# Optimization experiments

Measured on AMD Instinct MI355X. Metric: run time of the kernel, lower is better.

Reference implementation:

```python
import jax, jax.numpy as jnp
import numpy as np

N_NODES = 100000


def gcn_conv(x, src, dst, W, b, n):
    # PyG GCNConv: x' = D^-1/2 (A + I) D^-1/2 (x W) + b
    h = x @ W  # [N, out] transform first (cheaper when out < in)
    loop = jnp.arange(n, dtype=src.dtype)
    s = jnp.concatenate([src, loop])
    d = jnp.concatenate([dst, loop])
    deg = jax.ops.segment_sum(jnp.ones_like(s, dtype=h.dtype), d, num_segments=n)
    dinv = jnp.where(deg > 0, jax.lax.rsqrt(deg), 0.0)
    norm = dinv[s] * dinv[d]  # [E+N]
    msg = h[s] * norm[:, None]  # [E+N, out]
    agg = jax.ops.segment_sum(msg, d, num_segments=n)
    return agg + b


def setup_inputs() -> dict:
    key = jax.random.key(0)
    ks = jax.random.split(key, 12)
    n, E, labels = N_NODES, 1600000, 128
    edges = jax.random.randint(ks[0], (2, E), 0, n, dtype=jnp.int64)
    features = jax.random.normal(ks[1], (n, labels), dtype=jnp.float32)

    def kaiming(k, fan_in, shape):
        return jax.random.normal(k, shape, dtype=jnp.float32) * np.sqrt(2.0 / fan_in)

    return {
        "edges": edges,
        "features": features,
        "W1": kaiming(ks[2], labels, (labels, 64)),
        "b1": jnp.zeros((64,), jnp.float32),
        "W2": kaiming(ks[3], 64, (64, 32)),
        "b2": jnp.zeros((32,), jnp.float32),
        "W3": kaiming(ks[4], 32, (32, 16)),
        "b3": jnp.zeros((16,), jnp.float32),
        "Wfc": kaiming(ks[5], 112, (112, 16)),
        "bfc": jnp.zeros((16,), jnp.float32),
    }


def reference(edges, features, W1, b1, W2, b2, W3, b3, Wfc, bfc):
    n = features.shape[0]
    src, dst = edges[0], edges[1]
    # eval mode: dropout is identity
    f1 = jax.nn.relu(gcn_conv(features, src, dst, W1, b1, n))  # [N, 64]
    f2 = jax.nn.relu(gcn_conv(f1, src, dst, W2, b2, n))        # [N, 32]
    f3 = jax.nn.relu(gcn_conv(f2, src, dst, W3, b3, n))        # [N, 16]
    cat = jnp.concatenate([f1, f2, f3], axis=1)                 # [N, 112]
    return jax.nn.relu(cat @ Wfc + bfc)                         # [N, 16]
```

## Files before the change

### kernel.cpp

```cpp
#include <hip/hip_runtime.h>

#define THREADS 256

typedef unsigned short u16;
typedef float f32x4 __attribute__((ext_vector_type(4)));
typedef short bf16x8 __attribute__((ext_vector_type(8)));

constexpr int SH = 9;
constexpr int NB = 1 << SH;
constexpr int TILE = 4096;

__device__ inline float bf2f(u16 u) {
  union { unsigned int i; float f; } c;
  c.i = ((unsigned int)u) << 16;
  return c.f;
}
__device__ inline u16 f2bf(float f) {
  union { float f; unsigned int i; } c;
  c.f = f;
  unsigned int r = c.i + 0x7fff + ((c.i >> 16) & 1);
  return (u16)(r >> 16);
}

union V8 {
  bf16x8 v;
  short s[8];
  u16 u[8];
  ushort4 u4[2];
};


__global__ void __launch_bounds__(256) k_hist(const int* __restrict__ dst,
                                              int* __restrict__ ghist, int E,
                                              int nblk, int nbk) {
  __shared__ int lcnt[NB];
  int t = threadIdx.x, blk = blockIdx.x;
  for (int i = t; i < nbk; i += 256) lcnt[i] = 0;
  __syncthreads();
  int beg = blk * TILE, end = min(beg + TILE, E);
  for (int e = beg + t; e < end; e += 256) atomicAdd(&lcnt[dst[e] >> SH], 1);
  __syncthreads();
  for (int i = t; i < nbk; i += 256) ghist[i * nblk + blk] = lcnt[i];
}

__global__ void __launch_bounds__(256) k_scanA(int* __restrict__ ghist,
                                               int* __restrict__ bsum, int nblk) {
  __shared__ int sc[256];
  int i = blockIdx.x, t = threadIdx.x;
  int* row = ghist + (size_t)i * nblk;
  int e0 = 2 * t, e1 = 2 * t + 1;
  int a0 = (e0 < nblk) ? row[e0] : 0;
  int a1 = (e1 < nblk) ? row[e1] : 0;
  int s = a0 + a1;
  sc[t] = s;
  __syncthreads();
  for (int o = 1; o < 256; o <<= 1) {
    int x = (t >= o) ? sc[t - o] : 0;
    __syncthreads();
    sc[t] += x;
    __syncthreads();
  }
  int base = sc[t] - s;
  if (e0 < nblk) row[e0] = base;
  if (e1 < nblk) row[e1] = base + a0;
  if (t == 255) bsum[i] = sc[255];
}

__global__ void __launch_bounds__(256) k_scanB(const int* __restrict__ bsum,
                                               int* __restrict__ bbase, int nbk) {
  __shared__ int sc[256];
  int t = threadIdx.x;
  int v = (t < nbk) ? bsum[t] : 0;
  sc[t] = v;
  __syncthreads();
  for (int o = 1; o < 256; o <<= 1) {
    int x = (t >= o) ? sc[t - o] : 0;
    __syncthreads();
    sc[t] += x;
    __syncthreads();
  }
  if (t < nbk) bbase[t] = sc[t] - v;
}

__global__ void __launch_bounds__(256) k_part(const int* __restrict__ src,
                                              const int* __restrict__ dst,
                                              const int* __restrict__ goff,
                                              const int* __restrict__ bbase,
                                              int* __restrict__ ebuf, int E,
                                              int nblk, int nbk) {
  __shared__ int lcur[NB];
  int t = threadIdx.x, blk = blockIdx.x;
  for (int i = t; i < nbk; i += 256) lcur[i] = goff[(size_t)i * nblk + blk] + bbase[i];
  __syncthreads();
  int beg = blk * TILE, end = min(beg + TILE, E);
  for (int e = beg + t; e < end; e += 256) {
    int s = src[e], d = dst[e];
    int p = atomicAdd(&lcur[d >> SH], 1);
    ebuf[p] = s | ((d & (NB - 1)) << 20);
  }
}

__global__ void __launch_bounds__(256) k_refine(
    const int* __restrict__ ebuf, const int* __restrict__ goff,
    const int* __restrict__ bbase, int* __restrict__ rowptr,
    int* __restrict__ colsrc, float* __restrict__ dinv,
    int n, int nbk, int nblk, int E) {
  __shared__ int cnt[NB];
  __shared__ int cur[NB];
  __shared__ int sc[256];
  int b = blockIdx.x, t = threadIdx.x;
  int beg = goff[(size_t)b * nblk] + bbase[b];
  int end = (b + 1 < nbk) ? goff[(size_t)(b + 1) * nblk] + bbase[b + 1] : E;
  cnt[t] = 0;
  cnt[t + 256] = 0;
  __syncthreads();
  for (int i = beg + t; i < end; i += 256) atomicAdd(&cnt[ebuf[i] >> 20], 1);
  __syncthreads();
  int c0 = cnt[2 * t], c1 = cnt[2 * t + 1];
  int a = c0 + c1;
  sc[t] = a;
  __syncthreads();
  for (int o = 1; o < 256; o <<= 1) {
    int x = (t >= o) ? sc[t - o] : 0;
    __syncthreads();
    sc[t] += x;
    __syncthreads();
  }
  int base0 = beg + sc[t] - a;
  int base1 = base0 + c0;
  int node0 = b << SH;
  int n0 = node0 + 2 * t, n1 = n0 + 1;
  cur[2 * t] = base0;
  cur[2 * t + 1] = base1;
  if (n0 <= n) rowptr[n0] = base0;
  if (n1 <= n) rowptr[n1] = base1;
  if (n0 < n) dinv[n0] = rsqrtf((float)(c0 + 1));
  if (n1 < n) dinv[n1] = rsqrtf((float)(c1 + 1));
  __syncthreads();
  for (int i = beg + t; i < end; i += 256) {
    int w = ebuf[i];
    int p = atomicAdd(&cur[w >> 20], 1);
    colsrc[p] = w & 0xFFFFF;
  }
}


template <int KC, int FOUT, bool BF16IN>
__global__ void __launch_bounds__(256) k_xform(
    const void* __restrict__ xin, const float* __restrict__ Wg,
    const float* __restrict__ dinv, u16* __restrict__ g, int n) {
  constexpr int FIN = KC * 32;
  constexpr int NC = FOUT / 16;
  constexpr int ASLOTS = 8 * KC * 64;
  constexpr int WSLOTS = KC * NC * 64;
  __shared__ short xa[ASLOTS * 8];
  __shared__ short wb[WSLOTS * 8];

  int t = threadIdx.x;
  int r0 = blockIdx.x * 128;

  for (int s = t; s < WSLOTS; s += 256) {
    int lane = s & 63, q = s >> 6;
    int nc = q % NC, kc = q / NC;
    int col = nc * 16 + (lane & 15);
    int kr = kc * 32 + (lane >> 4) * 8;
    V8 v;
#pragma unroll
    for (int j = 0; j < 8; ++j) v.s[j] = (short)f2bf(Wg[(kr + j) * FOUT + col]);
    *(bf16x8*)&wb[s * 8] = v.v;
  }

  for (int s = t; s < ASLOTS; s += 256) {
    int lane = s & 63, q = s >> 6;
    int kc = q % KC, mtile = q / KC;
    int row = mtile * 16 + (lane & 15);
    int k = kc * 32 + (lane >> 4) * 8;
    int gr = r0 + row;
    V8 v;
    if (gr < n) {
      if constexpr (BF16IN) {
        v.v = *(const bf16x8*)((const u16*)xin + (size_t)gr * FIN + k);
      } else {
        const float* xf = (const float*)xin + (size_t)gr * FIN + k;
        float4 p = *(const float4*)xf;
        float4 q4 = *(const float4*)(xf + 4);
        v.s[0] = (short)f2bf(p.x); v.s[1] = (short)f2bf(p.y);
        v.s[2] = (short)f2bf(p.z); v.s[3] = (short)f2bf(p.w);
        v.s[4] = (short)f2bf(q4.x); v.s[5] = (short)f2bf(q4.y);
        v.s[6] = (short)f2bf(q4.z); v.s[7] = (short)f2bf(q4.w);
      }
    } else {
      for (int j = 0; j < 8; ++j) v.s[j] = 0;
    }
    *(bf16x8*)&xa[s * 8] = v.v;
  }
  __syncthreads();

  int ln = t & 63, wv = t >> 6;
  int m0 = wv * 2;

  bf16x8 bf[KC * NC];
#pragma unroll
  for (int i = 0; i < KC * NC; ++i) bf[i] = *(const bf16x8*)&wb[(i * 64 + ln) * 8];

  f32x4 acc[2][NC];
#pragma unroll
  for (int i = 0; i < 2; ++i)
#pragma unroll
    for (int j = 0; j < NC; ++j) acc[i][j] = {0.f, 0.f, 0.f, 0.f};

#pragma unroll
  for (int kc = 0; kc < KC; ++kc) {
    bf16x8 a0 = *(const bf16x8*)&xa[(((m0 + 0) * KC + kc) * 64 + ln) * 8];
    bf16x8 a1 = *(const bf16x8*)&xa[(((m0 + 1) * KC + kc) * 64 + ln) * 8];
#pragma unroll
    for (int nc = 0; nc < NC; ++nc) {
      acc[0][nc] = __builtin_amdgcn_mfma_f32_16x16x32_bf16(a0, bf[kc * NC + nc], acc[0][nc], 0, 0, 0);
      acc[1][nc] = __builtin_amdgcn_mfma_f32_16x16x32_bf16(a1, bf[kc * NC + nc], acc[1][nc], 0, 0, 0);
    }
  }

  int colb = ln & 15, rq = ln >> 4;
#pragma unroll
  for (int mt2 = 0; mt2 < 2; ++mt2) {
#pragma unroll
    for (int reg = 0; reg < 4; ++reg) {
      int gr = r0 + (m0 + mt2) * 16 + rq * 4 + reg;
      if (gr < n) {
        float di = dinv[gr];
#pragma unroll
        for (int nc = 0; nc < NC; ++nc)
          g[(size_t)gr * FOUT + nc * 16 + colb] = f2bf(acc[mt2][nc][reg] * di);
      }
    }
  }
}


template <int F>
__global__ void __launch_bounds__(256) k_gather_fin(
    const u16* __restrict__ g, const int* __restrict__ rowptr,
    const int* __restrict__ colsrc, const float* __restrict__ dinv,
    const float* __restrict__ bias, u16* __restrict__ fout, int n) {
  constexpr int LPG = F / 8;
  constexpr int G = 64 / LPG;
  int t = threadIdx.x;
  int ln = t & 63, wib = t >> 6;
  int lanein = ln % LPG, grp = ln / LPG;
  int f0 = lanein * 8;
  float bb[8];
#pragma unroll
  for (int j = 0; j < 8; ++j) bb[j] = bias[f0 + j];
  int gw = blockIdx.x * (blockDim.x >> 6) + wib;
  int nwaves = (gridDim.x * blockDim.x) >> 6;
  for (int node = gw * G + grp; node < n; node += nwaves * G) {
    int b = rowptr[node], e = rowptr[node + 1];
    float p0[8], p1[8], p2[8], p3[8];
    {
      V8 u;
      u.v = *(const bf16x8*)&g[(size_t)node * F + f0];
#pragma unroll
      for (int j = 0; j < 8; ++j) {
        p0[j] = bf2f(u.u[j]);
        p1[j] = 0.f; p2[j] = 0.f; p3[j] = 0.f;
      }
    }
    int i = b;
    for (; i + 4 <= e; i += 4) {
      int s0 = colsrc[i + 0], s1 = colsrc[i + 1];
      int s2 = colsrc[i + 2], s3 = colsrc[i + 3];
      V8 u0, u1, u2, u3;
      u0.v = *(const bf16x8*)&g[(size_t)s0 * F + f0];
      u1.v = *(const bf16x8*)&g[(size_t)s1 * F + f0];
      u2.v = *(const bf16x8*)&g[(size_t)s2 * F + f0];
      u3.v = *(const bf16x8*)&g[(size_t)s3 * F + f0];
#pragma unroll
      for (int j = 0; j < 8; ++j) {
        p0[j] += bf2f(u0.u[j]);
        p1[j] += bf2f(u1.u[j]);
        p2[j] += bf2f(u2.u[j]);
        p3[j] += bf2f(u3.u[j]);
      }
    }
    for (; i < e; ++i) {
      int s = colsrc[i];
      V8 u;
      u.v = *(const bf16x8*)&g[(size_t)s * F + f0];
#pragma unroll
      for (int j = 0; j < 8; ++j) p1[j] += bf2f(u.u[j]);
    }
    float di = dinv[node];
    V8 o;
#pragma unroll
    for (int j = 0; j < 8; ++j) {
      float a = (p0[j] + p1[j]) + (p2[j] + p3[j]);
      o.u[j] = f2bf(fmaxf(fmaf(a, di, bb[j]), 0.f));
    }
    *(bf16x8*)&fout[(size_t)node * F + f0] = o.v;
  }
}


__global__ void __launch_bounds__(256) k_fc(
    const u16* __restrict__ f1, const u16* __restrict__ f2,
    const u16* __restrict__ f3, const float* __restrict__ Wfc,
    const float* __restrict__ bfc, float* __restrict__ out, int n) {
  constexpr int KC = 4, FOUT = 16;
  constexpr int ASLOTS = 8 * KC * 64;
  constexpr int WSLOTS = KC * 64;
  __shared__ short xa[ASLOTS * 8];
  __shared__ short wb[WSLOTS * 8];

  int t = threadIdx.x;
  int r0 = blockIdx.x * 128;

  for (int s = t; s < WSLOTS; s += 256) {
    int lane = s & 63, kc = s >> 6;
    int col = lane & 15;
    int kr = kc * 32 + (lane >> 4) * 8;
    V8 v;
#pragma unroll
    for (int j = 0; j < 8; ++j)
      v.s[j] = (kr + j < 112) ? (short)f2bf(Wfc[(kr + j) * FOUT + col]) : (short)0;
    *(bf16x8*)&wb[s * 8] = v.v;
  }

  for (int s = t; s < ASLOTS; s += 256) {
    int lane = s & 63, q = s >> 6;
    int kc = q & 3, mtile = q >> 2;
    int row = mtile * 16 + (lane & 15);
    int k = kc * 32 + (lane >> 4) * 8;
    int gr = r0 + row;
    V8 v;
    if (gr < n && k < 112) {
      if (k < 64) v.v = *(const bf16x8*)&f1[(size_t)gr * 64 + k];
      else if (k < 96) v.v = *(const bf16x8*)&f2[(size_t)gr * 32 + (k - 64)];
      else v.v = *(const bf16x8*)&f3[(size_t)gr * 16 + (k - 96)];
    } else {
      for (int j = 0; j < 8; ++j) v.s[j] = 0;
    }
    *(bf16x8*)&xa[s * 8] = v.v;
  }
  __syncthreads();

  int ln = t & 63, wv = t >> 6;
  int m0 = wv * 2;

  bf16x8 bf[KC];
#pragma unroll
  for (int i = 0; i < KC; ++i) bf[i] = *(const bf16x8*)&wb[(i * 64 + ln) * 8];

  f32x4 acc[2] = {{0.f, 0.f, 0.f, 0.f}, {0.f, 0.f, 0.f, 0.f}};
#pragma unroll
  for (int kc = 0; kc < KC; ++kc) {
    bf16x8 a0 = *(const bf16x8*)&xa[(((m0 + 0) * KC + kc) * 64 + ln) * 8];
    bf16x8 a1 = *(const bf16x8*)&xa[(((m0 + 1) * KC + kc) * 64 + ln) * 8];
    acc[0] = __builtin_amdgcn_mfma_f32_16x16x32_bf16(a0, bf[kc], acc[0], 0, 0, 0);
    acc[1] = __builtin_amdgcn_mfma_f32_16x16x32_bf16(a1, bf[kc], acc[1], 0, 0, 0);
  }

  int colb = ln & 15, rq = ln >> 4;
  float bb = bfc[colb];
#pragma unroll
  for (int mt2 = 0; mt2 < 2; ++mt2) {
#pragma unroll
    for (int reg = 0; reg < 4; ++reg) {
      int gr = r0 + (m0 + mt2) * 16 + rq * 4 + reg;
      if (gr < n) out[(size_t)gr * 16 + colb] = fmaxf(acc[mt2][reg] + bb, 0.f);
    }
  }
}


extern "C" void kernel_launch(void* const* d_in, const int* in_sizes, int n_in,
                              void* d_out, int out_size, void* d_ws, size_t ws_size,
                              hipStream_t stream) {
  const int* edges = (const int*)d_in[0];
  const float* feat = (const float*)d_in[1];
  const float* W1 = (const float*)d_in[2];
  const float* b1 = (const float*)d_in[3];
  const float* W2 = (const float*)d_in[4];
  const float* b2 = (const float*)d_in[5];
  const float* W3 = (const float*)d_in[6];
  const float* b3 = (const float*)d_in[7];
  const float* Wfc = (const float*)d_in[8];
  const float* bfc = (const float*)d_in[9];
  float* out = (float*)d_out;

  const int E = in_sizes[0] / 2;
  const int n = in_sizes[1] / 128;
  const int* srcp = edges;
  const int* dstp = edges + E;
  const int nbk = (n + NB - 1) >> SH;
  const int nblk = (E + TILE - 1) / TILE;

  char* w = (char*)d_ws;
  auto carve = [&](size_t bytes) {
    void* p = (void*)w;
    w += (bytes + 255) & ~(size_t)255;
    return p;
  };
  int* ghist = (int*)carve((size_t)nbk * nblk * 4);
  int* bsum = (int*)carve(256 * 4);
  int* bbase = (int*)carve(256 * 4);
  int* rowptr = (int*)carve(((size_t)n + 1) * 4);
  float* dinv = (float*)carve((size_t)n * 4);
  int* colsrc = (int*)carve((size_t)E * 4);
  size_t big = (size_t)E * 4 > (size_t)n * 128 ? (size_t)E * 4 : (size_t)n * 128;
  void* shared_big = carve(big);
  int* ebuf = (int*)shared_big;
  u16* g = (u16*)shared_big;
  u16* f1 = (u16*)carve((size_t)n * 64 * 2);
  u16* f2 = (u16*)carve((size_t)n * 32 * 2);
  u16* f3 = (u16*)carve((size_t)n * 16 * 2);

  k_hist<<<nblk, 256, 0, stream>>>(dstp, ghist, E, nblk, nbk);
  k_scanA<<<nbk, 256, 0, stream>>>(ghist, bsum, nblk);
  k_scanB<<<1, 256, 0, stream>>>(bsum, bbase, nbk);
  k_part<<<nblk, 256, 0, stream>>>(srcp, dstp, ghist, bbase, ebuf, E, nblk, nbk);
  k_refine<<<nbk, 256, 0, stream>>>(ebuf, ghist, bbase, rowptr, colsrc, dinv, n, nbk, nblk, E);

  const int xb = (n + 127) / 128;

  k_xform<4, 64, false><<<xb, 256, 0, stream>>>(feat, W1, dinv, g, n);
  k_gather_fin<64><<<2048, 256, 0, stream>>>(g, rowptr, colsrc, dinv, b1, f1, n);

  k_xform<2, 32, true><<<xb, 256, 0, stream>>>(f1, W2, dinv, g, n);
  k_gather_fin<32><<<2048, 256, 0, stream>>>(g, rowptr, colsrc, dinv, b2, f2, n);

  k_xform<1, 16, true><<<xb, 256, 0, stream>>>(f2, W3, dinv, g, n);
  k_gather_fin<16><<<2048, 256, 0, stream>>>(g, rowptr, colsrc, dinv, b3, f3, n);

  k_fc<<<xb, 256, 0, stream>>>(f1, f2, f3, Wfc, bfc, out, n);
}
```

Baseline: 169.8 us.

## Fuse gather with next-layer transform and split FC accumulation into layers

Each layer's neighbor-gather now writes its activated output into shared memory and immediately runs MFMA for both the next layer's weight transform and that layer's slice of the final FC, accumulating into the output buffer across layers. This removes the f1/f2/f3 round trips through global memory and two xform launches plus the separate FC kernel. The single-block scanB is folded into k_part and k_refine, which each redo the small prefix scan, and rowptr[n] is set explicitly. The gather now uses fixed 128-row blocks instead of a grid-stride loop, which may hurt load balance. It also adds read-modify-write traffic on the output.

```diff
diff --git a/kernel.cpp b/kernel.cpp
--- a/kernel.cpp
+++ b/kernel.cpp
@@ -26,7 +26,6 @@
   bf16x8 v;
   short s[8];
   u16 u[8];
-  ushort4 u4[2];
 };
 
 
@@ -66,31 +65,26 @@
   if (t == 255) bsum[i] = sc[255];
 }
 
-__global__ void __launch_bounds__(256) k_scanB(const int* __restrict__ bsum,
-                                               int* __restrict__ bbase, int nbk) {
-  __shared__ int sc[256];
-  int t = threadIdx.x;
-  int v = (t < nbk) ? bsum[t] : 0;
-  sc[t] = v;
-  __syncthreads();
-  for (int o = 1; o < 256; o <<= 1) {
-    int x = (t >= o) ? sc[t - o] : 0;
-    __syncthreads();
-    sc[t] += x;
-    __syncthreads();
-  }
-  if (t < nbk) bbase[t] = sc[t] - v;
-}
-
 __global__ void __launch_bounds__(256) k_part(const int* __restrict__ src,
                                               const int* __restrict__ dst,
                                               const int* __restrict__ goff,
-                                              const int* __restrict__ bbase,
+                                              const int* __restrict__ bsum,
                                               int* __restrict__ ebuf, int E,
                                               int nblk, int nbk) {
   __shared__ int lcur[NB];
+  __shared__ int sb[256];
   int t = threadIdx.x, blk = blockIdx.x;
-  for (int i = t; i < nbk; i += 256) lcur[i] = goff[(size_t)i * nblk + blk] + bbase[i];
+  int v = (t < nbk) ? bsum[t] : 0;
+  sb[t] = v;
+  __syncthreads();
+  for (int o = 1; o < 256; o <<= 1) {
+    int x = (t >= o) ? sb[t - o] : 0;
+    __syncthreads();
+    sb[t] += x;
+    __syncthreads();
+  }
+  for (int i = t; i < nbk; i += 256)
+    lcur[i] = goff[(size_t)i * nblk + blk] + (i ? sb[i - 1] : 0);
   __syncthreads();
   int beg = blk * TILE, end = min(beg + TILE, E);
   for (int e = beg + t; e < end; e += 256) {
@@ -102,15 +96,27 @@
 
 __global__ void __launch_bounds__(256) k_refine(
     const int* __restrict__ ebuf, const int* __restrict__ goff,
-    const int* __restrict__ bbase, int* __restrict__ rowptr,
+    const int* __restrict__ bsum, int* __restrict__ rowptr,
     int* __restrict__ colsrc, float* __restrict__ dinv,
     int n, int nbk, int nblk, int E) {
   __shared__ int cnt[NB];
   __shared__ int cur[NB];
   __shared__ int sc[256];
+  __shared__ int bex[256];
   int b = blockIdx.x, t = threadIdx.x;
-  int beg = goff[(size_t)b * nblk] + bbase[b];
-  int end = (b + 1 < nbk) ? goff[(size_t)(b + 1) * nblk] + bbase[b + 1] : E;
+  {
+    int v = (t < nbk) ? bsum[t] : 0;
+    bex[t] = v;
+    __syncthreads();
+    for (int o = 1; o < 256; o <<= 1) {
+      int x = (t >= o) ? bex[t - o] : 0;
+      __syncthreads();
+      bex[t] += x;
+      __syncthreads();
+    }
+  }
+  int beg = goff[(size_t)b * nblk] + (b ? bex[b - 1] : 0);
+  int end = (b + 1 < nbk) ? goff[(size_t)(b + 1) * nblk] + bex[b] : E;
   cnt[t] = 0;
   cnt[t + 256] = 0;
   __syncthreads();
@@ -136,6 +142,7 @@
   if (n1 <= n) rowptr[n1] = base1;
   if (n0 < n) dinv[n0] = rsqrtf((float)(c0 + 1));
   if (n1 < n) dinv[n1] = rsqrtf((float)(c1 + 1));
+  if (b == nbk - 1 && t == 0) rowptr[n] = E;
   __syncthreads();
   for (int i = beg + t; i < end; i += 256) {
     int w = ebuf[i];
@@ -237,136 +244,179 @@
 }
 
 
-template <int F>
-__global__ void __launch_bounds__(256) k_gather_fin(
-    const u16* __restrict__ g, const int* __restrict__ rowptr,
+template <int GF, int GOUT, int FCROW0, int FCROWS, int MODE>
+__global__ void __launch_bounds__(256) k_gx(
+    const u16* __restrict__ gin, const int* __restrict__ rowptr,
     const int* __restrict__ colsrc, const float* __restrict__ dinv,
-    const float* __restrict__ bias, u16* __restrict__ fout, int n) {
-  constexpr int LPG = F / 8;
-  constexpr int G = 64 / LPG;
-  int t = threadIdx.x;
-  int ln = t & 63, wib = t >> 6;
-  int lanein = ln % LPG, grp = ln / LPG;
-  int f0 = lanein * 8;
-  float bb[8];
-#pragma unroll
-  for (int j = 0; j < 8; ++j) bb[j] = bias[f0 + j];
-  int gw = blockIdx.x * (blockDim.x >> 6) + wib;
-  int nwaves = (gridDim.x * blockDim.x) >> 6;
-  for (int node = gw * G + grp; node < n; node += nwaves * G) {
-    int b = rowptr[node], e = rowptr[node + 1];
-    float p0[8], p1[8], p2[8], p3[8];
-    {
-      V8 u;
-      u.v = *(const bf16x8*)&g[(size_t)node * F + f0];
-#pragma unroll
-      for (int j = 0; j < 8; ++j) {
-        p0[j] = bf2f(u.u[j]);
-        p1[j] = 0.f; p2[j] = 0.f; p3[j] = 0.f;
-      }
-    }
-    int i = b;
-    for (; i + 4 <= e; i += 4) {
-      int s0 = colsrc[i + 0], s1 = colsrc[i + 1];
-      int s2 = colsrc[i + 2], s3 = colsrc[i + 3];
-      V8 u0, u1, u2, u3;
-      u0.v = *(const bf16x8*)&g[(size_t)s0 * F + f0];
-      u1.v = *(const bf16x8*)&g[(size_t)s1 * F + f0];
-      u2.v = *(const bf16x8*)&g[(size_t)s2 * F + f0];
-      u3.v = *(const bf16x8*)&g[(size_t)s3 * F + f0];
-#pragma unroll
-      for (int j = 0; j < 8; ++j) {
-        p0[j] += bf2f(u0.u[j]);
-        p1[j] += bf2f(u1.u[j]);
-        p2[j] += bf2f(u2.u[j]);
-        p3[j] += bf2f(u3.u[j]);
-      }
-    }
-    for (; i < e; ++i) {
-      int s = colsrc[i];
-      V8 u;
-      u.v = *(const bf16x8*)&g[(size_t)s * F + f0];
-#pragma unroll
-      for (int j = 0; j < 8; ++j) p1[j] += bf2f(u.u[j]);
-    }
-    float di = dinv[node];
-    V8 o;
-#pragma unroll
-    for (int j = 0; j < 8; ++j) {
-      float a = (p0[j] + p1[j]) + (p2[j] + p3[j]);
-      o.u[j] = f2bf(fmaxf(fmaf(a, di, bb[j]), 0.f));
-    }
-    *(bf16x8*)&fout[(size_t)node * F + f0] = o.v;
-  }
-}
-
-
-__global__ void __launch_bounds__(256) k_fc(
-    const u16* __restrict__ f1, const u16* __restrict__ f2,
-    const u16* __restrict__ f3, const float* __restrict__ Wfc,
-    const float* __restrict__ bfc, float* __restrict__ out, int n) {
-  constexpr int KC = 4, FOUT = 16;
+    const float* __restrict__ bias, const float* __restrict__ Wg,
+    const float* __restrict__ Wfc, const float* __restrict__ bfc,
+    u16* __restrict__ gout, float* __restrict__ out, int n) {
+  constexpr int KC = (GF + 31) / 32;
+  constexpr int NCG = (GOUT > 0) ? (GOUT / 16) : 1;
   constexpr int ASLOTS = 8 * KC * 64;
-  constexpr int WSLOTS = KC * 64;
+  constexpr int WGSLOTS = (GOUT > 0) ? (KC * NCG * 64) : 64;
+  constexpr int WFSLOTS = KC * 64;
   __shared__ short xa[ASLOTS * 8];
-  __shared__ short wb[WSLOTS * 8];
+  __shared__ short wgb[WGSLOTS * 8];
+  __shared__ short wfb[WFSLOTS * 8];
 
   int t = threadIdx.x;
   int r0 = blockIdx.x * 128;
 
-  for (int s = t; s < WSLOTS; s += 256) {
+  {
+    V8 z;
+#pragma unroll
+    for (int j = 0; j < 8; ++j) z.s[j] = 0;
+    for (int s = t; s < ASLOTS; s += 256) *(bf16x8*)&xa[s * 8] = z.v;
+  }
+  if constexpr (GOUT > 0) {
+    for (int s = t; s < WGSLOTS; s += 256) {
+      int lane = s & 63, q = s >> 6;
+      int nc = q % NCG, kc = q / NCG;
+      int col = nc * 16 + (lane & 15);
+      int kr = kc * 32 + (lane >> 4) * 8;
+      V8 v;
+#pragma unroll
+      for (int j = 0; j < 8; ++j) v.s[j] = (short)f2bf(Wg[(kr + j) * GOUT + col]);
+      *(bf16x8*)&wgb[s * 8] = v.v;
+    }
+  }
+  for (int s = t; s < WFSLOTS; s += 256) {
     int lane = s & 63, kc = s >> 6;
     int col = lane & 15;
     int kr = kc * 32 + (lane >> 4) * 8;
     V8 v;
 #pragma unroll
     for (int j = 0; j < 8; ++j)
-      v.s[j] = (kr + j < 112) ? (short)f2bf(Wfc[(kr + j) * FOUT + col]) : (short)0;
-    *(bf16x8*)&wb[s * 8] = v.v;
-  }
-
-  for (int s = t; s < ASLOTS; s += 256) {
-    int lane = s & 63, q = s >> 6;
-    int kc = q & 3, mtile = q >> 2;
-    int row = mtile * 16 + (lane & 15);
-    int k = kc * 32 + (lane >> 4) * 8;
-    int gr = r0 + row;
-    V8 v;
-    if (gr < n && k < 112) {
-      if (k < 64) v.v = *(const bf16x8*)&f1[(size_t)gr * 64 + k];
-      else if (k < 96) v.v = *(const bf16x8*)&f2[(size_t)gr * 32 + (k - 64)];
-      else v.v = *(const bf16x8*)&f3[(size_t)gr * 16 + (k - 96)];
-    } else {
-      for (int j = 0; j < 8; ++j) v.s[j] = 0;
-    }
-    *(bf16x8*)&xa[s * 8] = v.v;
+      v.s[j] = (kr + j < FCROWS) ? (short)f2bf(Wfc[(FCROW0 + kr + j) * 16 + col]) : (short)0;
+    *(bf16x8*)&wfb[s * 8] = v.v;
+  }
+  __syncthreads();
+
+  {
+    constexpr int LPG = GF / 8;
+    constexpr int NPW = 64 / LPG;
+    constexpr int PASSES = 128 / (NPW * 4);
+    int ln = t & 63, wib = t >> 6;
+    int lanein = ln % LPG, grp = ln / LPG;
+    int f0 = lanein * 8;
+    float bb[8];
+#pragma unroll
+    for (int j = 0; j < 8; ++j) bb[j] = bias[f0 + j];
+#pragma unroll
+    for (int pass = 0; pass < PASSES; ++pass) {
+      int lr = pass * (NPW * 4) + wib * NPW + grp;
+      int gr = r0 + lr;
+      if (gr < n) {
+        int b = rowptr[gr], e = rowptr[gr + 1];
+        float p0[8], p1[8], p2[8], p3[8];
+        {
+          V8 u;
+          u.v = *(const bf16x8*)&gin[(size_t)gr * GF + f0];
+#pragma unroll
+          for (int j = 0; j < 8; ++j) {
+            p0[j] = bf2f(u.u[j]);
+            p1[j] = 0.f; p2[j] = 0.f; p3[j] = 0.f;
+          }
+        }
+        int i = b;
+        for (; i + 4 <= e; i += 4) {
+          int s0 = colsrc[i + 0], s1 = colsrc[i + 1];
+          int s2 = colsrc[i + 2], s3 = colsrc[i + 3];
+          V8 u0, u1, u2, u3;
+          u0.v = *(const bf16x8*)&gin[(size_t)s0 * GF + f0];
+          u1.v = *(const bf16x8*)&gin[(size_t)s1 * GF + f0];
+          u2.v = *(const bf16x8*)&gin[(size_t)s2 * GF + f0];
+          u3.v = *(const bf16x8*)&gin[(size_t)s3 * GF + f0];
+#pragma unroll
+          for (int j = 0; j < 8; ++j) {
+            p0[j] += bf2f(u0.u[j]);
+            p1[j] += bf2f(u1.u[j]);
+            p2[j] += bf2f(u2.u[j]);
+            p3[j] += bf2f(u3.u[j]);
+          }
+        }
+        for (; i < e; ++i) {
+          int s = colsrc[i];
+          V8 u;
+          u.v = *(const bf16x8*)&gin[(size_t)s * GF + f0];
+#pragma unroll
+          for (int j = 0; j < 8; ++j) p1[j] += bf2f(u.u[j]);
+        }
+        float di = dinv[gr];
+        V8 o;
+#pragma unroll
+        for (int j = 0; j < 8; ++j) {
+          float a = (p0[j] + p1[j]) + (p2[j] + p3[j]);
+          o.u[j] = f2bf(fmaxf(fmaf(a, di, bb[j]), 0.f));
+        }
+        int kc = f0 >> 5, q = (f0 >> 3) & 3;
+        int slot = ((lr >> 4) * KC + kc) * 64 + ((lr & 15) | (q << 4));
+        *(bf16x8*)&xa[slot * 8] = o.v;
+      }
+    }
   }
   __syncthreads();
 
   int ln = t & 63, wv = t >> 6;
   int m0 = wv * 2;
 
-  bf16x8 bf[KC];
-#pragma unroll
-  for (int i = 0; i < KC; ++i) bf[i] = *(const bf16x8*)&wb[(i * 64 + ln) * 8];
-
-  f32x4 acc[2] = {{0.f, 0.f, 0.f, 0.f}, {0.f, 0.f, 0.f, 0.f}};
+  bf16x8 wgf[KC * NCG];
+  if constexpr (GOUT > 0) {
+#pragma unroll
+    for (int i = 0; i < KC * NCG; ++i) wgf[i] = *(const bf16x8*)&wgb[(i * 64 + ln) * 8];
+  }
+  bf16x8 wff[KC];
+#pragma unroll
+  for (int i = 0; i < KC; ++i) wff[i] = *(const bf16x8*)&wfb[(i * 64 + ln) * 8];
+
+  f32x4 accG[2][NCG];
+  f32x4 accF[2];
+#pragma unroll
+  for (int i = 0; i < 2; ++i) {
+    accF[i] = {0.f, 0.f, 0.f, 0.f};
+#pragma unroll
+    for (int j = 0; j < NCG; ++j) accG[i][j] = {0.f, 0.f, 0.f, 0.f};
+  }
+
 #pragma unroll
   for (int kc = 0; kc < KC; ++kc) {
     bf16x8 a0 = *(const bf16x8*)&xa[(((m0 + 0) * KC + kc) * 64 + ln) * 8];
     bf16x8 a1 = *(const bf16x8*)&xa[(((m0 + 1) * KC + kc) * 64 + ln) * 8];
-    acc[0] = __builtin_amdgcn_mfma_f32_16x16x32_bf16(a0, bf[kc], acc[0], 0, 0, 0);
-    acc[1] = __builtin_amdgcn_mfma_f32_16x16x32_bf16(a1, bf[kc], acc[1], 0, 0, 0);
+    if constexpr (GOUT > 0) {
+#pragma unroll
+      for (int nc = 0; nc < NCG; ++nc) {
+        accG[0][nc] = __builtin_amdgcn_mfma_f32_16x16x32_bf16(a0, wgf[kc * NCG + nc], accG[0][nc], 0, 0, 0);
+        accG[1][nc] = __builtin_amdgcn_mfma_f32_16x16x32_bf16(a1, wgf[kc * NCG + nc], accG[1][nc], 0, 0, 0);
+      }
+    }
+    accF[0] = __builtin_amdgcn_mfma_f32_16x16x32_bf16(a0, wff[kc], accF[0], 0, 0, 0);
+    accF[1] = __builtin_amdgcn_mfma_f32_16x16x32_bf16(a1, wff[kc], accF[1], 0, 0, 0);
   }
 
   int colb = ln & 15, rq = ln >> 4;
-  float bb = bfc[colb];
 #pragma unroll
   for (int mt2 = 0; mt2 < 2; ++mt2) {
 #pragma unroll
     for (int reg = 0; reg < 4; ++reg) {
       int gr = r0 + (m0 + mt2) * 16 + rq * 4 + reg;
-      if (gr < n) out[(size_t)gr * 16 + colb] = fmaxf(acc[mt2][reg] + bb, 0.f);
+      if (gr < n) {
+        if constexpr (GOUT > 0) {
+          float di = dinv[gr];
+#pragma unroll
+          for (int nc = 0; nc < NCG; ++nc)
+            gout[(size_t)gr * GOUT + nc * 16 + colb] = f2bf(accG[mt2][nc][reg] * di);
+        }
+        float fcv = accF[mt2][reg];
+        size_t oi = (size_t)gr * 16 + colb;
+        if constexpr (MODE == 0) {
+          out[oi] = fcv;
+        } else if constexpr (MODE == 1) {
+          out[oi] += fcv;
+        } else {
+          out[oi] = fmaxf(out[oi] + fcv + bfc[colb], 0.f);
+        }
+      }
     }
   }
 }
@@ -402,34 +452,29 @@
   };
   int* ghist = (int*)carve((size_t)nbk * nblk * 4);
   int* bsum = (int*)carve(256 * 4);
-  int* bbase = (int*)carve(256 * 4);
   int* rowptr = (int*)carve(((size_t)n + 1) * 4);
   float* dinv = (float*)carve((size_t)n * 4);
   int* colsrc = (int*)carve((size_t)E * 4);
   size_t big = (size_t)E * 4 > (size_t)n * 128 ? (size_t)E * 4 : (size_t)n * 128;
   void* shared_big = carve(big);
   int* ebuf = (int*)shared_big;
-  u16* g = (u16*)shared_big;
-  u16* f1 = (u16*)carve((size_t)n * 64 * 2);
-  u16* f2 = (u16*)carve((size_t)n * 32 * 2);
-  u16* f3 = (u16*)carve((size_t)n * 16 * 2);
+  u16* g1 = (u16*)shared_big;
+  u16* g3 = (u16*)shared_big;
+  u16* g2 = (u16*)carve((size_t)n * 32 * 2);
 
   k_hist<<<nblk, 256, 0, stream>>>(dstp, ghist, E, nblk, nbk);
   k_scanA<<<nbk, 256, 0, stream>>>(ghist, bsum, nblk);
-  k_scanB<<<1, 256, 0, stream>>>(bsum, bbase, nbk);
-  k_part<<<nblk, 256, 0, stream>>>(srcp, dstp, ghist, bbase, ebuf, E, nblk, nbk);
-  k_refine<<<nbk, 256, 0, stream>>>(ebuf, ghist, bbase, rowptr, colsrc, dinv, n, nbk, nblk, E);
+  k_part<<<nblk, 256, 0, stream>>>(srcp, dstp, ghist, bsum, ebuf, E, nblk, nbk);
+  k_refine<<<nbk, 256, 0, stream>>>(ebuf, ghist, bsum, rowptr, colsrc, dinv, n, nbk, nblk, E);
 
   const int xb = (n + 127) / 128;
 
-  k_xform<4, 64, false><<<xb, 256, 0, stream>>>(feat, W1, dinv, g, n);
-  k_gather_fin<64><<<2048, 256, 0, stream>>>(g, rowptr, colsrc, dinv, b1, f1, n);
-
-  k_xform<2, 32, true><<<xb, 256, 0, stream>>>(f1, W2, dinv, g, n);
-  k_gather_fin<32><<<2048, 256, 0, stream>>>(g, rowptr, colsrc, dinv, b2, f2, n);
-
-  k_xform<1, 16, true><<<xb, 256, 0, stream>>>(f2, W3, dinv, g, n);
-  k_gather_fin<16><<<2048, 256, 0, stream>>>(g, rowptr, colsrc, dinv, b3, f3, n);
-
-  k_fc<<<xb, 256, 0, stream>>>(f1, f2, f3, Wfc, bfc, out, n);
-}
+  k_xform<4, 64, false><<<xb, 256, 0, stream>>>(feat, W1, dinv, g1, n);
+  k_gx<64, 32, 0, 64, 0><<<xb, 256, 0, stream>>>(
+      g1, rowptr, colsrc, dinv, b1, W2, Wfc, bfc, g2, out, n);
+  k_gx<32, 16, 64, 32, 1><<<xb, 256, 0, stream>>>(
+      g2, rowptr, colsrc, dinv, b2, W3, Wfc, bfc, g3, out, n);
+  k_gx<16, 0, 96, 16, 2><<<xb, 256, 0, stream>>>(
+      g3, rowptr, colsrc, dinv, b3, (const float*)nullptr, Wfc, bfc,
+      (u16*)nullptr, out, n);
+}
```

Measured after the change: 157.6 us. 7.2% less time.
